# Kernel optimization log

Hardware: AMD Instinct MI355X
Metric: run time of the kernel (lower is better)

## Reference

```python
import jax, jax.numpy as jnp
import numpy as np

N_NODES = 100000
N_EDGES = 3200000
D_IN = 256
D_OUT = 256


def setup_inputs() -> dict:
    key = jax.random.key(0)
    k1, k2, k3, k4, k5, k6 = jax.random.split(key, 6)
    bound = 1.0 / np.sqrt(D_OUT)
    x = jax.random.normal(k1, (N_NODES, D_IN), dtype=jnp.float32)
    weight = jax.random.uniform(k2, (D_IN, D_OUT), dtype=jnp.float32, minval=-bound, maxval=bound)
    bias = jax.random.uniform(k3, (D_OUT,), dtype=jnp.float32, minval=-bound, maxval=bound)
    edge_src = jax.random.randint(k4, (N_EDGES,), 0, N_NODES, dtype=jnp.int32)
    edge_dst = jax.random.randint(k5, (N_EDGES,), 0, N_NODES, dtype=jnp.int32)
    edge_weight = jax.random.uniform(k6, (N_EDGES,), dtype=jnp.float32)
    return {"x": x, "weight": weight, "bias": bias,
            "edge_src": edge_src, "edge_dst": edge_dst, "edge_weight": edge_weight}


def reference(x, weight, bias, edge_src, edge_dst, edge_weight):
    # XW = X @ W  -- dense GEMM, [N, D_out]
    xw = jnp.matmul(x, weight)
    # Z = A @ XW, A in COO: Z[dst] += w_e * XW[src]
    msgs = xw[edge_src] * edge_weight[:, None]          # [E, D_out] gather + scale
    z = jax.ops.segment_sum(msgs, edge_dst, num_segments=N_NODES)  # scatter-add
    return z + bias
```

## Files before the change

kernel.cpp:

```cpp
#include <hip/hip_runtime.h>
#include <hip/hip_bf16.h>
#include <stdint.h>

#define N_NODES 100000
#define N_EDGES 3200000
#define DDIM 256
#define NB 782
#define CAP 4800
#define BINBLK 4096
#define OCAP 65536
#define NOFS 132

typedef __attribute__((ext_vector_type(8))) short short8v;
typedef __attribute__((ext_vector_type(4))) float f32x4;

static __device__ __forceinline__ unsigned short f32_to_bf16_rne(float f) {
  unsigned u = __float_as_uint(f);
  unsigned rounded = u + 0x7FFFu + ((u >> 16) & 1u);
  return (unsigned short)(rounded >> 16);
}

static __device__ __forceinline__ float bf16_to_f32(unsigned short h) {
  return __uint_as_float((unsigned)h << 16);
}

static __device__ __forceinline__ float bfLO(unsigned v) { return __uint_as_float(v << 16); }
static __device__ __forceinline__ float bfHI(unsigned v) { return __uint_as_float(v & 0xFFFF0000u); }


__global__ __launch_bounds__(256) void k_bin(const int* __restrict__ src,
                                             const int* __restrict__ dst,
                                             const float* __restrict__ w,
                                             int* __restrict__ bcur,
                                             uint2* __restrict__ bin,
                                             uint4* __restrict__ ofl,
                                             int* __restrict__ oflcnt) {
  __shared__ int hist[NB];
  const int t = threadIdx.x;
  const int e0 = blockIdx.x * BINBLK;
  int n = N_EDGES - e0;
  if (n > BINBLK) n = BINBLK;
  for (int i = t; i < NB; i += 256) hist[i] = 0;
  __syncthreads();
  int myd[16];
#pragma unroll
  for (int j = 0; j < 16; ++j) {
    int p = j * 256 + t;
    if (p < n) {
      myd[j] = dst[e0 + p];
      atomicAdd(&hist[myd[j] >> 7], 1);
    } else {
      myd[j] = -1;
    }
  }
  __syncthreads();
  for (int i = t; i < NB; i += 256) {
    int h = hist[i];
    hist[i] = h ? atomicAdd(&bcur[i * 16], h) : 0;
  }
  __syncthreads();
#pragma unroll
  for (int j = 0; j < 16; ++j) {
    int p = j * 256 + t;
    if (p < n) {
      int d = myd[j];
      int bkt = d >> 7;
      int q = atomicAdd(&hist[bkt], 1);
      if (q < CAP) {
        bin[(size_t)bkt * CAP + q] =
            make_uint2(((unsigned)(d & 127) << 17) | (unsigned)src[e0 + p],
                       __float_as_uint(w[e0 + p]));
      } else {
        int op = atomicAdd(oflcnt, 1);
        if (op < OCAP)
          ofl[op] = make_uint4((unsigned)d, (unsigned)src[e0 + p],
                               __float_as_uint(w[e0 + p]), 0u);
      }
    }
  }
}


__global__ __launch_bounds__(512) void k_sort(const uint2* __restrict__ bin1,
                                              const int* __restrict__ bcur,
                                              uint2* __restrict__ bin2,
                                              int* __restrict__ nof) {
  __shared__ int lh[129];
  __shared__ int lc[128];
  const int b = blockIdx.x;
  const int t = threadIdx.x;
  int cnt = bcur[b * 16];
  if (cnt > CAP) cnt = CAP;
  if (t < 129) lh[t] = 0;
  __syncthreads();
  const int wid = t >> 6;
  const int lane = t & 63;
  uint2 rec[10];
  int nrec = 0;
#pragma unroll
  for (int j = 0; j < 10; ++j) {
    int p = t + j * 512;
    if (p < cnt) {
      rec[j] = bin1[(size_t)b * CAP + p];
      atomicAdd(&lh[(rec[j].x >> 17) + 1], 1);
      nrec = j + 1;
    }
  }
  __syncthreads();
  if (wid == 0) {
    int v0 = lh[lane + 1];
    int v1 = lh[lane + 65];
#pragma unroll
    for (int d = 1; d < 64; d <<= 1) {
      int u = __shfl_up(v0, d);
      if (lane >= d) v0 += u;
    }
    int tot0 = __shfl(v0, 63);
#pragma unroll
    for (int d = 1; d < 64; d <<= 1) {
      int u = __shfl_up(v1, d);
      if (lane >= d) v1 += u;
    }
    v1 += tot0;
    lh[lane + 1] = v0;
    lh[lane + 65] = v1;
  }
  __syncthreads();
  if (t < 128) lc[t] = lh[t];
  __syncthreads();
#pragma unroll
  for (int j = 0; j < 10; ++j) {
    if (j < nrec) {
      int q = atomicAdd(&lc[rec[j].x >> 17], 1);
      bin2[(size_t)b * CAP + q] = rec[j];
    }
  }
  if (t < 129) nof[b * NOFS + t] = lh[t];
}


__global__ __launch_bounds__(256) void k_cvtW(const float* __restrict__ w,
                                              unsigned short* __restrict__ wt) {
  int i = blockIdx.x * blockDim.x + threadIdx.x;
  int k = i >> 8;
  int n = i & 255;
  wt[(size_t)n * DDIM + k] = f32_to_bf16_rne(w[(size_t)k * DDIM + n]);
}


__global__ __launch_bounds__(512, 2) void k_gemm(const float* __restrict__ x,
                                                 const unsigned short* __restrict__ wt,
                                                 unsigned short* __restrict__ xw) {
  __shared__ unsigned short As[128 * 64];
  __shared__ unsigned short Bs[256 * 64];
  const int t = threadIdx.x;
  const int lane = t & 63;
  const int wid = t >> 6;
  const int wr = wid >> 1;
  const int wc = wid & 1;
  const int m0 = blockIdx.x * 128;

  f32x4 acc[2][8] = {};

  const int arow = t >> 2;
  const int akb = (t & 3) * 16;
  int am = m0 + arow;
  if (am > N_NODES - 1) am = N_NODES - 1;
  const int sr = t >> 3;
  const int sc = t & 7;

  const int kg = lane >> 4;
  const int rl = lane & 15;

  for (int kt = 0; kt < 4; ++kt) {
    const int k0 = kt * 64;
#pragma unroll
    for (int i = 0; i < 4; ++i) {
      int r = i * 64 + sr;
      int cc = sc ^ (r & 7);
      const unsigned short* srcp = wt + (size_t)r * DDIM + k0 + cc * 8;
      __builtin_amdgcn_global_load_lds(
          (const __attribute__((address_space(1))) void*)srcp,
          (__attribute__((address_space(3))) void*)((char*)Bs + i * 8192 + t * 16),
          16, 0, 0);
    }
    {
      const float* xp = x + (size_t)am * DDIM + k0 + akb;
      float4 f0 = *(const float4*)(xp + 0);
      float4 f1 = *(const float4*)(xp + 4);
      float4 f2 = *(const float4*)(xp + 8);
      float4 f3 = *(const float4*)(xp + 12);
      uint4 p0, p1;
      p0.x = (unsigned)f32_to_bf16_rne(f0.x) | ((unsigned)f32_to_bf16_rne(f0.y) << 16);
      p0.y = (unsigned)f32_to_bf16_rne(f0.z) | ((unsigned)f32_to_bf16_rne(f0.w) << 16);
      p0.z = (unsigned)f32_to_bf16_rne(f1.x) | ((unsigned)f32_to_bf16_rne(f1.y) << 16);
      p0.w = (unsigned)f32_to_bf16_rne(f1.z) | ((unsigned)f32_to_bf16_rne(f1.w) << 16);
      p1.x = (unsigned)f32_to_bf16_rne(f2.x) | ((unsigned)f32_to_bf16_rne(f2.y) << 16);
      p1.y = (unsigned)f32_to_bf16_rne(f2.z) | ((unsigned)f32_to_bf16_rne(f2.w) << 16);
      p1.z = (unsigned)f32_to_bf16_rne(f3.x) | ((unsigned)f32_to_bf16_rne(f3.y) << 16);
      p1.w = (unsigned)f32_to_bf16_rne(f3.z) | ((unsigned)f32_to_bf16_rne(f3.w) << 16);
      int b0 = arow * 128 + akb * 2;
      int swz = (arow & 7) << 4;
      *(uint4*)((char*)As + (b0 ^ swz)) = p0;
      *(uint4*)((char*)As + ((b0 + 16) ^ swz)) = p1;
    }
    __syncthreads();

#pragma unroll
    for (int ks = 0; ks < 2; ++ks) {
      const int colbyte = ks * 64 + kg * 16;
      short8v af[2];
#pragma unroll
      for (int mi = 0; mi < 2; ++mi) {
        int row = wr * 32 + mi * 16 + rl;
        int b = row * 128 + (colbyte ^ ((row & 7) << 4));
        af[mi] = *(const short8v*)((const char*)As + b);
      }
#pragma unroll
      for (int ni = 0; ni < 8; ++ni) {
        int row = wc * 128 + ni * 16 + rl;
        int b = row * 128 + (colbyte ^ ((row & 7) << 4));
        short8v bf = *(const short8v*)((const char*)Bs + b);
        acc[0][ni] = __builtin_amdgcn_mfma_f32_16x16x32_bf16(af[0], bf, acc[0][ni], 0, 0, 0);
        acc[1][ni] = __builtin_amdgcn_mfma_f32_16x16x32_bf16(af[1], bf, acc[1][ni], 0, 0, 0);
      }
    }
    __syncthreads();
  }

  const int rbase = (lane >> 4) * 4;
  const int ncol = lane & 15;
#pragma unroll
  for (int mi = 0; mi < 2; ++mi) {
#pragma unroll
    for (int ni = 0; ni < 8; ++ni) {
      int n = wc * 128 + ni * 16 + ncol;
#pragma unroll
      for (int r = 0; r < 4; ++r) {
        int m = m0 + wr * 32 + mi * 16 + rbase + r;
        if (m < N_NODES)
          xw[(size_t)m * DDIM + n] = f32_to_bf16_rne(acc[mi][ni][r]);
      }
    }
  }
}


__global__ __launch_bounds__(256, 8) void k_baggr(const uint2* __restrict__ bin2,
                                                  const int* __restrict__ nof,
                                                  const unsigned short* __restrict__ xw,
                                                  const float* __restrict__ bias,
                                                  float* __restrict__ z) {
  const int b = blockIdx.x;
  const int q = blockIdx.y & 3;
  const int h = blockIdx.y >> 2;
  const int t = threadIdx.x;
  const int wid = t >> 6;
  const int lane = t & 63;
  const int g = lane >> 3;
  const int l8 = lane & 7;
  const int gofs = q * 64 + l8 * 8;
  const uint2* mybin = bin2 + (size_t)b * CAP;
  const int* myof = nof + b * NOFS + h * 64;

  float4 bv = make_float4(0.f, 0.f, 0.f, 0.f);
  if (g < 2) bv = *(const float4*)(bias + gofs + (g ? 4 : 0));

#pragma unroll 1
  for (int ii = 0; ii < 16; ++ii) {
    const int i = wid * 16 + ii;
    const int node = (b << 7) + h * 64 + i;
    if (node >= N_NODES) break;
    const int s = myof[i];
    const int e2 = myof[i + 1];
    float a0 = 0.f, a1 = 0.f, a2 = 0.f, a3 = 0.f;
    float a4 = 0.f, a5 = 0.f, a6 = 0.f, a7 = 0.f;
#pragma unroll 1
    for (int p = s; p < e2; p += 32) {
      unsigned sx0, sx1, sx2, sx3;
      float w0, w1, w2, w3;
      {
        int i0 = p + 0 * 8 + g; bool k0 = i0 < e2; uint2 r = mybin[k0 ? i0 : s];
        sx0 = r.x & 0x1FFFFu; w0 = k0 ? __uint_as_float(r.y) : 0.f;
      }
      {
        int i1 = p + 1 * 8 + g; bool k1 = i1 < e2; uint2 r = mybin[k1 ? i1 : s];
        sx1 = r.x & 0x1FFFFu; w1 = k1 ? __uint_as_float(r.y) : 0.f;
      }
      {
        int i2 = p + 2 * 8 + g; bool k2 = i2 < e2; uint2 r = mybin[k2 ? i2 : s];
        sx2 = r.x & 0x1FFFFu; w2 = k2 ? __uint_as_float(r.y) : 0.f;
      }
      {
        int i3 = p + 3 * 8 + g; bool k3 = i3 < e2; uint2 r = mybin[k3 ? i3 : s];
        sx3 = r.x & 0x1FFFFu; w3 = k3 ? __uint_as_float(r.y) : 0.f;
      }
      uint4 v0 = *(const uint4*)(xw + (size_t)sx0 * DDIM + gofs);
      uint4 v1 = *(const uint4*)(xw + (size_t)sx1 * DDIM + gofs);
      uint4 v2 = *(const uint4*)(xw + (size_t)sx2 * DDIM + gofs);
      uint4 v3 = *(const uint4*)(xw + (size_t)sx3 * DDIM + gofs);
      a0 += w0 * bfLO(v0.x); a1 += w0 * bfHI(v0.x);
      a2 += w0 * bfLO(v0.y); a3 += w0 * bfHI(v0.y);
      a4 += w0 * bfLO(v0.z); a5 += w0 * bfHI(v0.z);
      a6 += w0 * bfLO(v0.w); a7 += w0 * bfHI(v0.w);
      a0 += w1 * bfLO(v1.x); a1 += w1 * bfHI(v1.x);
      a2 += w1 * bfLO(v1.y); a3 += w1 * bfHI(v1.y);
      a4 += w1 * bfLO(v1.z); a5 += w1 * bfHI(v1.z);
      a6 += w1 * bfLO(v1.w); a7 += w1 * bfHI(v1.w);
      a0 += w2 * bfLO(v2.x); a1 += w2 * bfHI(v2.x);
      a2 += w2 * bfLO(v2.y); a3 += w2 * bfHI(v2.y);
      a4 += w2 * bfLO(v2.z); a5 += w2 * bfHI(v2.z);
      a6 += w2 * bfLO(v2.w); a7 += w2 * bfHI(v2.w);
      a0 += w3 * bfLO(v3.x); a1 += w3 * bfHI(v3.x);
      a2 += w3 * bfLO(v3.y); a3 += w3 * bfHI(v3.y);
      a4 += w3 * bfLO(v3.z); a5 += w3 * bfHI(v3.z);
      a6 += w3 * bfLO(v3.w); a7 += w3 * bfHI(v3.w);
    }
    a0 += __shfl_xor(a0, 8); a0 += __shfl_xor(a0, 16); a0 += __shfl_xor(a0, 32);
    a1 += __shfl_xor(a1, 8); a1 += __shfl_xor(a1, 16); a1 += __shfl_xor(a1, 32);
    a2 += __shfl_xor(a2, 8); a2 += __shfl_xor(a2, 16); a2 += __shfl_xor(a2, 32);
    a3 += __shfl_xor(a3, 8); a3 += __shfl_xor(a3, 16); a3 += __shfl_xor(a3, 32);
    a4 += __shfl_xor(a4, 8); a4 += __shfl_xor(a4, 16); a4 += __shfl_xor(a4, 32);
    a5 += __shfl_xor(a5, 8); a5 += __shfl_xor(a5, 16); a5 += __shfl_xor(a5, 32);
    a6 += __shfl_xor(a6, 8); a6 += __shfl_xor(a6, 16); a6 += __shfl_xor(a6, 32);
    a7 += __shfl_xor(a7, 8); a7 += __shfl_xor(a7, 16); a7 += __shfl_xor(a7, 32);
    if (g < 2) {
      float4 o = g ? make_float4(a4 + bv.x, a5 + bv.y, a6 + bv.z, a7 + bv.w)
                   : make_float4(a0 + bv.x, a1 + bv.y, a2 + bv.z, a3 + bv.w);
      *(float4*)(z + (size_t)node * DDIM + gofs + (g ? 4 : 0)) = o;
    }
  }
}


__global__ __launch_bounds__(256) void k_ofl(const uint4* __restrict__ ofl,
                                             const int* __restrict__ oflcnt,
                                             const unsigned short* __restrict__ xw,
                                             float* __restrict__ z) {
  int n = oflcnt[0];
  if (n > OCAP) n = OCAP;
  for (int r = blockIdx.x; r < n; r += gridDim.x) {
    uint4 rec = ofl[r];
    float wgt = __uint_as_float(rec.z);
    int c = threadIdx.x;
    float v = bf16_to_f32(xw[(size_t)rec.y * DDIM + c]);
    atomicAdd(&z[(size_t)rec.x * DDIM + c], wgt * v);
  }
}

extern "C" void kernel_launch(void* const* d_in, const int* in_sizes, int n_in,
                              void* d_out, int out_size, void* d_ws, size_t ws_size,
                              hipStream_t stream) {
  const float* x = (const float*)d_in[0];
  const float* w = (const float*)d_in[1];
  const float* bias = (const float*)d_in[2];
  const int* esrc = (const int*)d_in[3];
  const int* edst = (const int*)d_in[4];
  const float* ew = (const float*)d_in[5];
  float* z = (float*)d_out;

  char* ws = (char*)d_ws;
  size_t off = 0;
  unsigned short* xw = (unsigned short*)(ws + off);
  off += (size_t)N_NODES * DDIM * 2;
  unsigned short* wt = (unsigned short*)(ws + off);
  off += (size_t)DDIM * DDIM * 2;
  int* bcur = (int*)(ws + off);
  off += (size_t)NB * 16 * 4;
  int* oflcnt = (int*)(ws + off);
  off += 256;
  int* nof = (int*)(ws + off);
  off += (size_t)NB * NOFS * 4;
  uint4* ofl = (uint4*)(ws + off);
  off += (size_t)OCAP * 16;
  uint2* bin1 = (uint2*)(ws + off);
  off += (size_t)NB * CAP * 8;
  uint2* bin2 = (uint2*)(ws + off);
  off += (size_t)NB * CAP * 8;

  hipMemsetAsync(bcur, 0, (size_t)NB * 16 * 4 + 256, stream);
  k_bin<<<(N_EDGES + BINBLK - 1) / BINBLK, 256, 0, stream>>>(esrc, edst, ew, bcur, bin1,
                                                             ofl, oflcnt);
  k_sort<<<NB, 512, 0, stream>>>(bin1, bcur, bin2, nof);
  k_cvtW<<<(DDIM * DDIM + 255) / 256, 256, 0, stream>>>(w, wt);
  k_gemm<<<(N_NODES + 127) / 128, 512, 0, stream>>>(x, wt, xw);
  dim3 ag(NB, 8);
  k_baggr<<<ag, 256, 0, stream>>>(bin2, nof, xw, bias, z);
  k_ofl<<<64, 256, 0, stream>>>(ofl, oflcnt, xw, z);
}
```

Baseline: 451.9 us.

## Co-schedule GEMM and edge binning in one kernel; stage bins in LDS for aggregation

Measured after the change: 374.5 us. 17.1% less time.

```diff
diff --git a/kernel.cpp b/kernel.cpp
--- a/kernel.cpp
+++ b/kernel.cpp
@@ -10,6 +10,7 @@
 #define BINBLK 4096
 #define OCAP 65536
 #define NOFS 132
+#define LCAP 2432
 
 typedef __attribute__((ext_vector_type(8))) short short8v;
 typedef __attribute__((ext_vector_type(4))) float f32x4;
@@ -28,53 +29,163 @@
 static __device__ __forceinline__ float bfHI(unsigned v) { return __uint_as_float(v & 0xFFFF0000u); }
 
 
-__global__ __launch_bounds__(256) void k_bin(const int* __restrict__ src,
-                                             const int* __restrict__ dst,
-                                             const float* __restrict__ w,
-                                             int* __restrict__ bcur,
-                                             uint2* __restrict__ bin,
-                                             uint4* __restrict__ ofl,
-                                             int* __restrict__ oflcnt) {
-  __shared__ int hist[NB];
+__global__ __launch_bounds__(256) void k_cvtW(const float* __restrict__ w,
+                                              unsigned short* __restrict__ wt) {
+  int i = blockIdx.x * blockDim.x + threadIdx.x;
+  int k = i >> 8;
+  int n = i & 255;
+  wt[(size_t)n * DDIM + k] = f32_to_bf16_rne(w[(size_t)k * DDIM + n]);
+}
+
+
+__global__ __launch_bounds__(512, 2) void k_gb(const float* __restrict__ x,
+                                               const unsigned short* __restrict__ wt,
+                                               unsigned short* __restrict__ xw,
+                                               const int* __restrict__ esrc,
+                                               const int* __restrict__ edst,
+                                               const float* __restrict__ ew,
+                                               int* __restrict__ bcur,
+                                               uint2* __restrict__ bin,
+                                               uint4* __restrict__ ofl,
+                                               int* __restrict__ oflcnt) {
+  __shared__ __align__(16) char smem[48 * 1024];
   const int t = threadIdx.x;
-  const int e0 = blockIdx.x * BINBLK;
-  int n = N_EDGES - e0;
-  if (n > BINBLK) n = BINBLK;
-  for (int i = t; i < NB; i += 256) hist[i] = 0;
-  __syncthreads();
-  int myd[16];
-#pragma unroll
-  for (int j = 0; j < 16; ++j) {
-    int p = j * 256 + t;
-    if (p < n) {
-      myd[j] = dst[e0 + p];
-      atomicAdd(&hist[myd[j] >> 7], 1);
-    } else {
-      myd[j] = -1;
-    }
-  }
-  __syncthreads();
-  for (int i = t; i < NB; i += 256) {
-    int h = hist[i];
-    hist[i] = h ? atomicAdd(&bcur[i * 16], h) : 0;
-  }
-  __syncthreads();
-#pragma unroll
-  for (int j = 0; j < 16; ++j) {
-    int p = j * 256 + t;
-    if (p < n) {
-      int d = myd[j];
-      int bkt = d >> 7;
-      int q = atomicAdd(&hist[bkt], 1);
-      if (q < CAP) {
-        bin[(size_t)bkt * CAP + q] =
-            make_uint2(((unsigned)(d & 127) << 17) | (unsigned)src[e0 + p],
-                       __float_as_uint(w[e0 + p]));
+  const int sub = blockIdx.x >> 1;
+
+  if ((blockIdx.x & 1) == 0) {
+    unsigned short* As = (unsigned short*)smem;
+    unsigned short* Bs = (unsigned short*)(smem + 16384);
+    const int lane = t & 63;
+    const int wid = t >> 6;
+    const int wr = wid >> 1;
+    const int wc = wid & 1;
+    const int m0 = sub * 128;
+
+    f32x4 acc[2][8] = {};
+
+    const int arow = t >> 2;
+    const int akb = (t & 3) * 16;
+    int am = m0 + arow;
+    if (am > N_NODES - 1) am = N_NODES - 1;
+    const int sr = t >> 3;
+    const int sc = t & 7;
+
+    const int kg = lane >> 4;
+    const int rl = lane & 15;
+
+    for (int kt = 0; kt < 4; ++kt) {
+      const int k0 = kt * 64;
+#pragma unroll
+      for (int i = 0; i < 4; ++i) {
+        int r = i * 64 + sr;
+        int cc = sc ^ (r & 7);
+        const unsigned short* srcp = wt + (size_t)r * DDIM + k0 + cc * 8;
+        __builtin_amdgcn_global_load_lds(
+            (const __attribute__((address_space(1))) void*)srcp,
+            (__attribute__((address_space(3))) void*)((char*)Bs + i * 8192 + t * 16),
+            16, 0, 0);
+      }
+      {
+        const float* xp = x + (size_t)am * DDIM + k0 + akb;
+        float4 f0 = *(const float4*)(xp + 0);
+        float4 f1 = *(const float4*)(xp + 4);
+        float4 f2 = *(const float4*)(xp + 8);
+        float4 f3 = *(const float4*)(xp + 12);
+        uint4 p0, p1;
+        p0.x = (unsigned)f32_to_bf16_rne(f0.x) | ((unsigned)f32_to_bf16_rne(f0.y) << 16);
+        p0.y = (unsigned)f32_to_bf16_rne(f0.z) | ((unsigned)f32_to_bf16_rne(f0.w) << 16);
+        p0.z = (unsigned)f32_to_bf16_rne(f1.x) | ((unsigned)f32_to_bf16_rne(f1.y) << 16);
+        p0.w = (unsigned)f32_to_bf16_rne(f1.z) | ((unsigned)f32_to_bf16_rne(f1.w) << 16);
+        p1.x = (unsigned)f32_to_bf16_rne(f2.x) | ((unsigned)f32_to_bf16_rne(f2.y) << 16);
+        p1.y = (unsigned)f32_to_bf16_rne(f2.z) | ((unsigned)f32_to_bf16_rne(f2.w) << 16);
+        p1.z = (unsigned)f32_to_bf16_rne(f3.x) | ((unsigned)f32_to_bf16_rne(f3.y) << 16);
+        p1.w = (unsigned)f32_to_bf16_rne(f3.z) | ((unsigned)f32_to_bf16_rne(f3.w) << 16);
+        int b0 = arow * 128 + akb * 2;
+        int swz = (arow & 7) << 4;
+        *(uint4*)((char*)As + (b0 ^ swz)) = p0;
+        *(uint4*)((char*)As + ((b0 + 16) ^ swz)) = p1;
+      }
+      __syncthreads();
+
+#pragma unroll
+      for (int ks = 0; ks < 2; ++ks) {
+        const int colbyte = ks * 64 + kg * 16;
+        short8v af[2];
+#pragma unroll
+        for (int mi = 0; mi < 2; ++mi) {
+          int row = wr * 32 + mi * 16 + rl;
+          int bo = row * 128 + (colbyte ^ ((row & 7) << 4));
+          af[mi] = *(const short8v*)((const char*)As + bo);
+        }
+#pragma unroll
+        for (int ni = 0; ni < 8; ++ni) {
+          int row = wc * 128 + ni * 16 + rl;
+          int bo = row * 128 + (colbyte ^ ((row & 7) << 4));
+          short8v bf = *(const short8v*)((const char*)Bs + bo);
+          acc[0][ni] = __builtin_amdgcn_mfma_f32_16x16x32_bf16(af[0], bf, acc[0][ni], 0, 0, 0);
+          acc[1][ni] = __builtin_amdgcn_mfma_f32_16x16x32_bf16(af[1], bf, acc[1][ni], 0, 0, 0);
+        }
+      }
+      __syncthreads();
+    }
+
+    const int rbase = (lane >> 4) * 4;
+    const int ncol = lane & 15;
+#pragma unroll
+    for (int mi = 0; mi < 2; ++mi) {
+#pragma unroll
+      for (int ni = 0; ni < 8; ++ni) {
+        int n = wc * 128 + ni * 16 + ncol;
+#pragma unroll
+        for (int r = 0; r < 4; ++r) {
+          int m = m0 + wr * 32 + mi * 16 + rbase + r;
+          if (m < N_NODES)
+            xw[(size_t)m * DDIM + n] = f32_to_bf16_rne(acc[mi][ni][r]);
+        }
+      }
+    }
+  } else {
+    int* hist = (int*)smem;
+    const int e0 = sub * BINBLK;
+    int n = N_EDGES - e0;
+    if (n > BINBLK) n = BINBLK;
+    if (n < 0) n = 0;
+    for (int i = t; i < NB; i += 512) hist[i] = 0;
+    __syncthreads();
+    int myd[8];
+#pragma unroll
+    for (int j = 0; j < 8; ++j) {
+      int p = j * 512 + t;
+      if (p < n) {
+        myd[j] = edst[e0 + p];
+        atomicAdd(&hist[myd[j] >> 7], 1);
       } else {
-        int op = atomicAdd(oflcnt, 1);
-        if (op < OCAP)
-          ofl[op] = make_uint4((unsigned)d, (unsigned)src[e0 + p],
-                               __float_as_uint(w[e0 + p]), 0u);
+        myd[j] = -1;
+      }
+    }
+    __syncthreads();
+    for (int i = t; i < NB; i += 512) {
+      int h = hist[i];
+      hist[i] = h ? atomicAdd(&bcur[i * 16], h) : 0;
+    }
+    __syncthreads();
+#pragma unroll
+    for (int j = 0; j < 8; ++j) {
+      int p = j * 512 + t;
+      if (p < n) {
+        int d = myd[j];
+        int bkt = d >> 7;
+        int q = atomicAdd(&hist[bkt], 1);
+        if (q < CAP) {
+          bin[(size_t)bkt * CAP + q] =
+              make_uint2(((unsigned)(d & 127) << 17) | (unsigned)esrc[e0 + p],
+                         __float_as_uint(ew[e0 + p]));
+        } else {
+          int op = atomicAdd(oflcnt, 1);
+          if (op < OCAP)
+            ofl[op] = make_uint4((unsigned)d, (unsigned)esrc[e0 + p],
+                                 __float_as_uint(ew[e0 + p]), 0u);
+        }
       }
     }
   }
@@ -139,166 +250,74 @@
 }
 
 
-__global__ __launch_bounds__(256) void k_cvtW(const float* __restrict__ w,
-                                              unsigned short* __restrict__ wt) {
-  int i = blockIdx.x * blockDim.x + threadIdx.x;
-  int k = i >> 8;
-  int n = i & 255;
-  wt[(size_t)n * DDIM + k] = f32_to_bf16_rne(w[(size_t)k * DDIM + n]);
-}
-
-
-__global__ __launch_bounds__(512, 2) void k_gemm(const float* __restrict__ x,
-                                                 const unsigned short* __restrict__ wt,
-                                                 unsigned short* __restrict__ xw) {
-  __shared__ unsigned short As[128 * 64];
-  __shared__ unsigned short Bs[256 * 64];
-  const int t = threadIdx.x;
-  const int lane = t & 63;
-  const int wid = t >> 6;
-  const int wr = wid >> 1;
-  const int wc = wid & 1;
-  const int m0 = blockIdx.x * 128;
-
-  f32x4 acc[2][8] = {};
-
-  const int arow = t >> 2;
-  const int akb = (t & 3) * 16;
-  int am = m0 + arow;
-  if (am > N_NODES - 1) am = N_NODES - 1;
-  const int sr = t >> 3;
-  const int sc = t & 7;
-
-  const int kg = lane >> 4;
-  const int rl = lane & 15;
-
-  for (int kt = 0; kt < 4; ++kt) {
-    const int k0 = kt * 64;
-#pragma unroll
-    for (int i = 0; i < 4; ++i) {
-      int r = i * 64 + sr;
-      int cc = sc ^ (r & 7);
-      const unsigned short* srcp = wt + (size_t)r * DDIM + k0 + cc * 8;
-      __builtin_amdgcn_global_load_lds(
-          (const __attribute__((address_space(1))) void*)srcp,
-          (__attribute__((address_space(3))) void*)((char*)Bs + i * 8192 + t * 16),
-          16, 0, 0);
-    }
-    {
-      const float* xp = x + (size_t)am * DDIM + k0 + akb;
-      float4 f0 = *(const float4*)(xp + 0);
-      float4 f1 = *(const float4*)(xp + 4);
-      float4 f2 = *(const float4*)(xp + 8);
-      float4 f3 = *(const float4*)(xp + 12);
-      uint4 p0, p1;
-      p0.x = (unsigned)f32_to_bf16_rne(f0.x) | ((unsigned)f32_to_bf16_rne(f0.y) << 16);
-      p0.y = (unsigned)f32_to_bf16_rne(f0.z) | ((unsigned)f32_to_bf16_rne(f0.w) << 16);
-      p0.z = (unsigned)f32_to_bf16_rne(f1.x) | ((unsigned)f32_to_bf16_rne(f1.y) << 16);
-      p0.w = (unsigned)f32_to_bf16_rne(f1.z) | ((unsigned)f32_to_bf16_rne(f1.w) << 16);
-      p1.x = (unsigned)f32_to_bf16_rne(f2.x) | ((unsigned)f32_to_bf16_rne(f2.y) << 16);
-      p1.y = (unsigned)f32_to_bf16_rne(f2.z) | ((unsigned)f32_to_bf16_rne(f2.w) << 16);
-      p1.z = (unsigned)f32_to_bf16_rne(f3.x) | ((unsigned)f32_to_bf16_rne(f3.y) << 16);
-      p1.w = (unsigned)f32_to_bf16_rne(f3.z) | ((unsigned)f32_to_bf16_rne(f3.w) << 16);
-      int b0 = arow * 128 + akb * 2;
-      int swz = (arow & 7) << 4;
-      *(uint4*)((char*)As + (b0 ^ swz)) = p0;
-      *(uint4*)((char*)As + ((b0 + 16) ^ swz)) = p1;
-    }
-    __syncthreads();
-
-#pragma unroll
-    for (int ks = 0; ks < 2; ++ks) {
-      const int colbyte = ks * 64 + kg * 16;
-      short8v af[2];
-#pragma unroll
-      for (int mi = 0; mi < 2; ++mi) {
-        int row = wr * 32 + mi * 16 + rl;
-        int b = row * 128 + (colbyte ^ ((row & 7) << 4));
-        af[mi] = *(const short8v*)((const char*)As + b);
-      }
-#pragma unroll
-      for (int ni = 0; ni < 8; ++ni) {
-        int row = wc * 128 + ni * 16 + rl;
-        int b = row * 128 + (colbyte ^ ((row & 7) << 4));
-        short8v bf = *(const short8v*)((const char*)Bs + b);
-        acc[0][ni] = __builtin_amdgcn_mfma_f32_16x16x32_bf16(af[0], bf, acc[0][ni], 0, 0, 0);
-        acc[1][ni] = __builtin_amdgcn_mfma_f32_16x16x32_bf16(af[1], bf, acc[1][ni], 0, 0, 0);
-      }
-    }
-    __syncthreads();
-  }
-
-  const int rbase = (lane >> 4) * 4;
-  const int ncol = lane & 15;
-#pragma unroll
-  for (int mi = 0; mi < 2; ++mi) {
-#pragma unroll
-    for (int ni = 0; ni < 8; ++ni) {
-      int n = wc * 128 + ni * 16 + ncol;
-#pragma unroll
-      for (int r = 0; r < 4; ++r) {
-        int m = m0 + wr * 32 + mi * 16 + rbase + r;
-        if (m < N_NODES)
-          xw[(size_t)m * DDIM + n] = f32_to_bf16_rne(acc[mi][ni][r]);
-      }
-    }
-  }
-}
-
-
 __global__ __launch_bounds__(256, 8) void k_baggr(const uint2* __restrict__ bin2,
                                                   const int* __restrict__ nof,
                                                   const unsigned short* __restrict__ xw,
                                                   const float* __restrict__ bias,
                                                   float* __restrict__ z) {
+  __shared__ uint2 lsrt[LCAP];
   const int b = blockIdx.x;
-  const int q = blockIdx.y & 3;
-  const int h = blockIdx.y >> 2;
+  const int h = blockIdx.y & 1;
+  const int c128 = (blockIdx.y >> 1) * 128;
   const int t = threadIdx.x;
   const int wid = t >> 6;
   const int lane = t & 63;
-  const int g = lane >> 3;
-  const int l8 = lane & 7;
-  const int gofs = q * 64 + l8 * 8;
+  const int g = lane >> 4;
+  const int l16 = lane & 15;
+  const int gofs = c128 + l16 * 8;
+  const int* myof = nof + b * NOFS + h * 64;
   const uint2* mybin = bin2 + (size_t)b * CAP;
-  const int* myof = nof + b * NOFS + h * 64;
+
+  const int base = myof[0];
+  const int cnth = myof[64] - base;
+  const uint2* rp;
+  int rbase;
+  if (cnth <= LCAP) {
+    for (int i = t; i < cnth; i += 256) lsrt[i] = mybin[base + i];
+    rp = (const uint2*)lsrt;
+    rbase = base;
+  } else {
+    rp = mybin;
+    rbase = 0;
+  }
+  __syncthreads();
 
   float4 bv = make_float4(0.f, 0.f, 0.f, 0.f);
-  if (g < 2) bv = *(const float4*)(bias + gofs + (g ? 4 : 0));
+  if (g < 2) bv = *(const float4*)(bias + gofs + g * 4);
 
 #pragma unroll 1
   for (int ii = 0; ii < 16; ++ii) {
     const int i = wid * 16 + ii;
     const int node = (b << 7) + h * 64 + i;
     if (node >= N_NODES) break;
-    const int s = myof[i];
-    const int e2 = myof[i + 1];
+    const int s = myof[i] - rbase;
+    const int e2 = myof[i + 1] - rbase;
     float a0 = 0.f, a1 = 0.f, a2 = 0.f, a3 = 0.f;
     float a4 = 0.f, a5 = 0.f, a6 = 0.f, a7 = 0.f;
 #pragma unroll 1
-    for (int p = s; p < e2; p += 32) {
+    for (int p = s; p < e2; p += 16) {
       unsigned sx0, sx1, sx2, sx3;
       float w0, w1, w2, w3;
       {
-        int i0 = p + 0 * 8 + g; bool k0 = i0 < e2; uint2 r = mybin[k0 ? i0 : s];
+        int i0 = p + 0 * 4 + g; bool k0 = i0 < e2; uint2 r = rp[k0 ? i0 : s];
         sx0 = r.x & 0x1FFFFu; w0 = k0 ? __uint_as_float(r.y) : 0.f;
       }
       {
-        int i1 = p + 1 * 8 + g; bool k1 = i1 < e2; uint2 r = mybin[k1 ? i1 : s];
+        int i1 = p + 1 * 4 + g; bool k1 = i1 < e2; uint2 r = rp[k1 ? i1 : s];
         sx1 = r.x & 0x1FFFFu; w1 = k1 ? __uint_as_float(r.y) : 0.f;
       }
       {
-        int i2 = p + 2 * 8 + g; bool k2 = i2 < e2; uint2 r = mybin[k2 ? i2 : s];
+        int i2 = p + 2 * 4 + g; bool k2 = i2 < e2; uint2 r = rp[k2 ? i2 : s];
         sx2 = r.x & 0x1FFFFu; w2 = k2 ? __uint_as_float(r.y) : 0.f;
       }
       {
-        int i3 = p + 3 * 8 + g; bool k3 = i3 < e2; uint2 r = mybin[k3 ? i3 : s];
+        int i3 = p + 3 * 4 + g; bool k3 = i3 < e2; uint2 r = rp[k3 ? i3 : s];
         sx3 = r.x & 0x1FFFFu; w3 = k3 ? __uint_as_float(r.y) : 0.f;
       }
-      uint4 v0 = *(const uint4*)(xw + (size_t)sx0 * DDIM + gofs);
-      uint4 v1 = *(const uint4*)(xw + (size_t)sx1 * DDIM + gofs);
-      uint4 v2 = *(const uint4*)(xw + (size_t)sx2 * DDIM + gofs);
-      uint4 v3 = *(const uint4*)(xw + (size_t)sx3 * DDIM + gofs);
+      uint4 v0 = *(const uint4*)(xw + ((sx0 << 8) + gofs));
+      uint4 v1 = *(const uint4*)(xw + ((sx1 << 8) + gofs));
+      uint4 v2 = *(const uint4*)(xw + ((sx2 << 8) + gofs));
+      uint4 v3 = *(const uint4*)(xw + ((sx3 << 8) + gofs));
       a0 += w0 * bfLO(v0.x); a1 += w0 * bfHI(v0.x);
       a2 += w0 * bfLO(v0.y); a3 += w0 * bfHI(v0.y);
       a4 += w0 * bfLO(v0.z); a5 += w0 * bfHI(v0.z);
@@ -316,18 +335,18 @@
       a4 += w3 * bfLO(v3.z); a5 += w3 * bfHI(v3.z);
       a6 += w3 * bfLO(v3.w); a7 += w3 * bfHI(v3.w);
     }
-    a0 += __shfl_xor(a0, 8); a0 += __shfl_xor(a0, 16); a0 += __shfl_xor(a0, 32);
-    a1 += __shfl_xor(a1, 8); a1 += __shfl_xor(a1, 16); a1 += __shfl_xor(a1, 32);
-    a2 += __shfl_xor(a2, 8); a2 += __shfl_xor(a2, 16); a2 += __shfl_xor(a2, 32);
-    a3 += __shfl_xor(a3, 8); a3 += __shfl_xor(a3, 16); a3 += __shfl_xor(a3, 32);
-    a4 += __shfl_xor(a4, 8); a4 += __shfl_xor(a4, 16); a4 += __shfl_xor(a4, 32);
-    a5 += __shfl_xor(a5, 8); a5 += __shfl_xor(a5, 16); a5 += __shfl_xor(a5, 32);
-    a6 += __shfl_xor(a6, 8); a6 += __shfl_xor(a6, 16); a6 += __shfl_xor(a6, 32);
-    a7 += __shfl_xor(a7, 8); a7 += __shfl_xor(a7, 16); a7 += __shfl_xor(a7, 32);
+    a0 += __shfl_xor(a0, 16); a0 += __shfl_xor(a0, 32);
+    a1 += __shfl_xor(a1, 16); a1 += __shfl_xor(a1, 32);
+    a2 += __shfl_xor(a2, 16); a2 += __shfl_xor(a2, 32);
+    a3 += __shfl_xor(a3, 16); a3 += __shfl_xor(a3, 32);
+    a4 += __shfl_xor(a4, 16); a4 += __shfl_xor(a4, 32);
+    a5 += __shfl_xor(a5, 16); a5 += __shfl_xor(a5, 32);
+    a6 += __shfl_xor(a6, 16); a6 += __shfl_xor(a6, 32);
+    a7 += __shfl_xor(a7, 16); a7 += __shfl_xor(a7, 32);
     if (g < 2) {
       float4 o = g ? make_float4(a4 + bv.x, a5 + bv.y, a6 + bv.z, a7 + bv.w)
                    : make_float4(a0 + bv.x, a1 + bv.y, a2 + bv.z, a3 + bv.w);
-      *(float4*)(z + (size_t)node * DDIM + gofs + (g ? 4 : 0)) = o;
+      *(float4*)(z + (size_t)node * DDIM + gofs + g * 4) = o;
     }
   }
 }
@@ -379,12 +398,10 @@
   off += (size_t)NB * CAP * 8;
 
   hipMemsetAsync(bcur, 0, (size_t)NB * 16 * 4 + 256, stream);
-  k_bin<<<(N_EDGES + BINBLK - 1) / BINBLK, 256, 0, stream>>>(esrc, edst, ew, bcur, bin1,
-                                                             ofl, oflcnt);
+  k_cvtW<<<(DDIM * DDIM + 255) / 256, 256, 0, stream>>>(w, wt);
+  k_gb<<<2 * NB, 512, 0, stream>>>(x, wt, xw, esrc, edst, ew, bcur, bin1, ofl, oflcnt);
   k_sort<<<NB, 512, 0, stream>>>(bin1, bcur, bin2, nof);
-  k_cvtW<<<(DDIM * DDIM + 255) / 256, 256, 0, stream>>>(w, wt);
-  k_gemm<<<(N_NODES + 127) / 128, 512, 0, stream>>>(x, wt, xw);
-  dim3 ag(NB, 8);
+  dim3 ag(NB, 4);
   k_baggr<<<ag, 256, 0, stream>>>(bin2, nof, xw, bias, z);
   k_ofl<<<64, 256, 0, stream>>>(ofl, oflcnt, xw, z);
 }
```
